# Performance work log

Hardware: AMD Instinct MI355X
Metric: run time of the kernel (lower is better)

## Reference

```python
import jax, jax.numpy as jnp
import numpy as np

B, C, H, W = 4, 128, 128, 128
_PARAM_IDS = ["1", "2", "4", "5", "7", "8", "9", "10", "12", "13", "15", "16"]


def setup_inputs() -> dict:
    key = jax.random.key(0)
    ks = jax.random.split(key, 2 + 2 * len(_PARAM_IDS))
    scale = 1.0 / np.sqrt(C).astype(np.float32)
    inp = {
        "x": jax.random.normal(ks[0], (B, C, H, W), jnp.float32),
        "y": jax.random.uniform(ks[1], (B, C, H, W), jnp.float32),  # edge gate in [0,1)
    }
    for i, n in enumerate(_PARAM_IDS):
        inp[f"w{n}"] = jax.random.normal(ks[2 + 2 * i], (C, C), jnp.float32) * scale
        inp[f"b{n}"] = jax.random.normal(ks[3 + 2 * i], (C,), jnp.float32) * scale
    return inp


def pw(t, w, b):
    # kernel-size-1 Conv1d: t [B,C,M] -> [B,C,M]
    return jnp.einsum('oc,bcm->bom', w, t) + b[None, :, None]


def gated_scan(seq_x, seq_y, wa, ba, wb, bb, relu_first):
    # seq_x, seq_y: [L, B, C, M]; recurrence h_k = relu(conv_a(x_k) + conv_b(h_{k-1}) * y_{k-1})
    first = jax.nn.relu(seq_x[0]) if relu_first else seq_x[0]

    def step(prev, inp):
        xi, yp = inp
        h = jax.nn.relu(pw(xi, wa, ba) + pw(prev, wb, bb) * yp)
        return h, h

    _, outs = jax.lax.scan(step, first, (seq_x[1:], seq_y[:-1]))
    return jnp.concatenate([first[None], outs], axis=0)


def reference(x, y, w1, b1, w2, b2, w4, b4, w5, b5, w7, b7, w8, b8,
              w9, b9, w10, b10, w12, b12, w13, b13, w15, b15, w16, b16):
    rows_x = jnp.transpose(x, (2, 0, 1, 3))   # [H,B,C,W]
    rows_y = jnp.transpose(y, (2, 0, 1, 3))   # [H,B,C,W]
    y_cols = jnp.transpose(y, (3, 0, 1, 2))   # [W,B,C,H]

    # south scan over height (row 0 untouched, no relu on it)
    hs_rows = gated_scan(rows_x, rows_y, w1, b1, w2, b2, relu_first=False)
    hs_cols = jnp.transpose(hs_rows, (3, 1, 2, 0))  # [W,B,C,H]
    # south-east / south-west scans over width (boundary column gets relu)
    hse = gated_scan(hs_cols, y_cols, w4, b4, w5, b5, relu_first=True)
    hsw = gated_scan(hs_cols[::-1], y_cols[::-1], w7, b7, w8, b8, relu_first=True)[::-1]

    # north scan over height (reversed; boundary row gets relu)
    hn_rows = gated_scan(rows_x[::-1], rows_y[::-1], w9, b9, w10, b10, relu_first=True)[::-1]
    hn_cols = jnp.transpose(hn_rows, (3, 1, 2, 0))  # [W,B,C,H]
    hne = gated_scan(hn_cols, y_cols, w12, b12, w13, b13, relu_first=True)
    hnw = gated_scan(hn_cols[::-1], y_cols[::-1], w15, b15, w16, b16, relu_first=True)[::-1]

    out_cols = hse + hsw + hne + hnw  # [W,B,C,H]
    return jnp.transpose(out_cols, (1, 2, 3, 0))  # [B,C,H,W]
```

## Files before the change

### kernel.cpp

```cpp
#include <hip/hip_runtime.h>

typedef unsigned int uint;
typedef unsigned short ushort;
typedef __attribute__((ext_vector_type(8))) short short8;
typedef __attribute__((ext_vector_type(4))) float f32x4;

#define NPOS 16384
#define PLANE 2097152
#define XR_OFF 0
#define GR_OFF 32768
#define OR_OFF 65536
#define HP_OFF 98304
#define LDS_BYTES 114688

__device__ __forceinline__ uint fbits(float a) { return __builtin_bit_cast(uint, a); }
__device__ __forceinline__ uint rnehi(float a) {
  const uint u = fbits(a);
  return (u + 0x7FFFu + ((u >> 16) & 1u)) & 0xFFFF0000u;
}
__device__ __forceinline__ float fhi(float a) { return __builtin_bit_cast(float, rnehi(a)); }
__device__ __forceinline__ uint packhi(float a, float b) { return (rnehi(a) >> 16) | rnehi(b); }
__device__ __forceinline__ uint packtr(float a, float b) {
  return (fbits(a) >> 16) | (fbits(b) & 0xFFFF0000u);
}
__device__ __forceinline__ float b2f(uint h16) { return __builtin_bit_cast(float, h16 << 16); }

__device__ __forceinline__ f32x4 MF(short8 a, short8 b, f32x4 c) {
  return __builtin_amdgcn_mfma_f32_16x16x32_bf16(a, b, c, 0, 0, 0);
}
__device__ __forceinline__ void fill16(const void* g, char* l) {
  __builtin_amdgcn_global_load_lds((const __attribute__((address_space(1))) void*)g,
                                   (__attribute__((address_space(3))) void*)l, 16, 0, 0);
}
__device__ __forceinline__ void split8(float4 v0, float4 v1, short8& hi, short8& lo) {
  union { short8 s; uint u[4]; } H, L;
  H.u[0] = packhi(v0.x, v0.y); H.u[1] = packhi(v0.z, v0.w);
  H.u[2] = packhi(v1.x, v1.y); H.u[3] = packhi(v1.z, v1.w);
  L.u[0] = packtr(v0.x - fhi(v0.x), v0.y - fhi(v0.y));
  L.u[1] = packtr(v0.z - fhi(v0.z), v0.w - fhi(v0.w));
  L.u[2] = packtr(v1.x - fhi(v1.x), v1.y - fhi(v1.y));
  L.u[3] = packtr(v1.z - fhi(v1.z), v1.w - fhi(v1.w));
  hi = H.s; lo = L.s;
}

#define BAR() asm volatile("s_waitcnt lgkmcnt(0)\n\ts_barrier" ::: "memory")


__global__ __launch_bounds__(256) void k_transpose_x(const float* __restrict__ x,
                                                     ushort* __restrict__ xhi,
                                                     ushort* __restrict__ xlo) {
  __shared__ float tile[128][129];
  const int b = blockIdx.x >> 7, h = blockIdx.x & 127;
  const int t = threadIdx.x, half = t >> 7, lane = t & 127;
  const float* src = x + (size_t)b * PLANE + (size_t)h * 128;
  for (int c0 = 0; c0 < 128; c0 += 2) {
    const int c = c0 + half;
    tile[c][lane] = src[(size_t)c * NPOS + lane];
  }
  __syncthreads();
  const int wq = t >> 6, cp = t & 63;
  for (int w0 = 0; w0 < 128; w0 += 4) {
    const int w = w0 + wq;
    const float v0 = tile[2 * cp][w], v1 = tile[2 * cp + 1][w];
    const size_t e = ((size_t)(b * 128 + w) * 128 + h) * 128 + 2 * cp;
    *(uint*)(xhi + e) = packhi(v0, v1);
    *(uint*)(xlo + e) = packtr(v0 - fhi(v0), v1 - fhi(v1));
  }
}

__global__ __launch_bounds__(256) void k_transpose_y(const float* __restrict__ y,
                                                     float* __restrict__ yt1,
                                                     float* __restrict__ yt2) {
  __shared__ float tile[128][129];
  const int b = blockIdx.x >> 7, h = blockIdx.x & 127;
  const int t = threadIdx.x, half = t >> 7, lane = t & 127;
  const float* src = y + (size_t)b * PLANE + (size_t)h * 128;
  for (int c0 = 0; c0 < 128; c0 += 2) {
    const int c = c0 + half;
    tile[c][lane] = src[(size_t)c * NPOS + lane];
  }
  __syncthreads();
  float* d1 = yt1 + (size_t)b * PLANE + (size_t)h * 128;
  float* d2 = yt2 + ((size_t)(b * 128 + h)) * NPOS;
  for (int w0 = 0; w0 < 128; w0 += 2) {
    const int w = w0 + half;
    const float v = tile[lane][w];
    d1[(size_t)w * NPOS + lane] = v;
    d2[(size_t)w * 128 + lane] = v;
  }
}

template <bool RELU0, bool REV, bool ACCUM, bool OUT16>
__device__ __forceinline__ void scan16(
    char* lds,
    const ushort* __restrict__ xhi, const ushort* __restrict__ xlo, size_t in_base,
    const float* __restrict__ gate, size_t gate_base,
    float* __restrict__ outf, ushort* __restrict__ outhi, ushort* __restrict__ outlo,
    size_t out_base, int out_ps, int out_ls,
    const float* __restrict__ Wa, const float* __restrict__ Ba,
    const float* __restrict__ Wb, const float* __restrict__ Bb) {
  const int t = threadIdx.x;
  const int wv = t >> 6, l = t & 63;
  const int line = l & 15, g4 = l >> 4;

  short8 wah[2][4], wal[2][4], wbh[2][4], wbl[2][4];
#pragma unroll
  for (int tt = 0; tt < 2; ++tt)
#pragma unroll
    for (int kt = 0; kt < 4; ++kt) {
      const int row = 32 * wv + 16 * tt + line;
      const int kc = 32 * kt + 8 * g4;
      const float4 a0 = *(const float4*)(Wa + row * 128 + kc);
      const float4 a1 = *(const float4*)(Wa + row * 128 + kc + 4);
      const float4 c0 = *(const float4*)(Wb + row * 128 + kc);
      const float4 c1 = *(const float4*)(Wb + row * 128 + kc + 4);
      split8(a0, a1, wah[tt][kt], wal[tt][kt]);
      split8(c0, c1, wbh[tt][kt], wbl[tt][kt]);
    }
  f32x4 baf[2], bbf[2];
#pragma unroll
  for (int tt = 0; tt < 2; ++tt) {
    baf[tt] = *(const f32x4*)(Ba + 32 * wv + 16 * tt + 4 * g4);
    bbf[tt] = *(const f32x4*)(Bb + 32 * wv + 16 * tt + 4 * g4);
  }

  auto P = [](int p) -> int { return REV ? 127 - p : p; };

  auto fillX = [&](int p, int slot) {
    const ushort* src = (wv >> 1) ? xlo : xhi;
#pragma unroll
    for (int kk = 0; kk < 2; ++kk) {
      const int k = 2 * (wv & 1) + kk;
      const int lf = 4 * k + g4;
      const int cf = l & 15;
      const size_t e = in_base + (size_t)lf * NPOS + (size_t)p * 128 + 8 * (cf ^ (lf & 7));
      fill16(src + e, lds + XR_OFF + slot * 8192 + (wv >> 1) * 4096 + k * 1024 + l * 16);
    }
  };
  auto fillG = [&](int p, int slot) {
#pragma unroll
    for (int kk = 0; kk < 2; ++kk) {
      const int k = 2 * wv + kk;
      const int lf = 2 * k + (l >> 5);
      const int cf = l & 31;
      const size_t e = gate_base + (size_t)lf * NPOS + (size_t)p * 128 + 4 * (cf ^ (lf & 7));
      fill16(gate + e, lds + GR_OFF + slot * 8192 + k * 1024 + l * 16);
    }
  };
  auto fillO = [&](int p, int slot) {
#pragma unroll
    for (int kk = 0; kk < 2; ++kk) {
      const int k = 2 * wv + kk;
      const int lf = 2 * k + (l >> 5);
      const int cf = l & 31;
      const size_t e = out_base + (size_t)p * out_ps + (size_t)lf * out_ls + 4 * (cf ^ (lf & 7));
      fill16(outf + e, lds + OR_OFF + slot * 8192 + k * 1024 + l * 16);
    }
  };

#pragma unroll
  for (int p = 0; p < 4; ++p) {
    fillX(P(p), p);
    fillG(P(p), p);
    if (ACCUM) fillO(P(p), p);
  }
  asm volatile("s_waitcnt vmcnt(0) lgkmcnt(0)\n\ts_barrier" ::: "memory");

  {
    const char* X0 = lds + XR_OFF;
    const char* O0 = lds + OR_OFF;
    char* Hwr = lds + HP_OFF;
#pragma unroll
    for (int tt = 0; tt < 2; ++tt) {
      const int chw = 4 * wv + 2 * tt + (g4 >> 1);
      const int boff = line * 256 + ((chw ^ (line & 7)) << 4) + 8 * (g4 & 1);
      const uint2 xh = *(const uint2*)(X0 + boff);
      const uint2 xl = *(const uint2*)(X0 + 4096 + boff);
      float4 f;
      f.x = b2f(xh.x & 0xFFFFu) + b2f(xl.x & 0xFFFFu);
      f.y = b2f(xh.x >> 16) + b2f(xl.x >> 16);
      f.z = b2f(xh.y & 0xFFFFu) + b2f(xl.y & 0xFFFFu);
      f.w = b2f(xh.y >> 16) + b2f(xl.y >> 16);
      if (RELU0) {
        f.x = fmaxf(f.x, 0.f); f.y = fmaxf(f.y, 0.f);
        f.z = fmaxf(f.z, 0.f); f.w = fmaxf(f.w, 0.f);
      }
      uint2 hw, lw;
      hw.x = packhi(f.x, f.y); hw.y = packhi(f.z, f.w);
      lw.x = packtr(f.x - fhi(f.x), f.y - fhi(f.y));
      lw.y = packtr(f.z - fhi(f.z), f.w - fhi(f.w));
      *(uint2*)(Hwr + boff) = hw;
      *(uint2*)(Hwr + 4096 + boff) = lw;
      const int ci0 = 32 * wv + 16 * tt + 4 * g4;
      const size_t oe = out_base + (size_t)P(0) * out_ps + (size_t)line * out_ls + ci0;
      if (OUT16) {
        *(uint2*)(outhi + oe) = hw;
        *(uint2*)(outlo + oe) = lw;
      } else {
        float4 o = f;
        if (ACCUM) {
          const int c32 = 8 * wv + 4 * tt + g4;
          const float4 ov = *(const float4*)(O0 + line * 512 + ((c32 ^ (line & 7)) << 4));
          o.x += ov.x; o.y += ov.y; o.z += ov.z; o.w += ov.w;
        }
        *(float4*)(outf + oe) = o;
      }
    }
  }
  BAR();

#pragma unroll 1
  for (int s = 1; s < 128; ++s) {
    if (s + 3 <= 127) {
      fillX(P(s + 3), (s + 3) & 3);
      if (ACCUM) fillO(P(s + 3), (s + 3) & 3);
    }
    if (s + 2 <= 127) fillG(P(s + 2), (s + 2) & 3);

    f32x4 accF[2], accR[2];
    accF[0] = baf[0]; accF[1] = baf[1];
    accR[0] = bbf[0]; accR[1] = bbf[1];
    const char* Hrd = lds + HP_OFF + ((s - 1) & 1) * 8192;
    const char* Xrd = lds + XR_OFF + (s & 3) * 8192;
#pragma unroll
    for (int kt = 0; kt < 4; ++kt) {
      const int ro = line * 256 + (((4 * kt + g4) ^ (line & 7)) << 4);
      const short8 hh = *(const short8*)(Hrd + ro);
      const short8 hl = *(const short8*)(Hrd + 4096 + ro);
      const short8 xh = *(const short8*)(Xrd + ro);
      const short8 xl = *(const short8*)(Xrd + 4096 + ro);
      accR[0] = MF(wbh[0][kt], hh, accR[0]);
      accR[0] = MF(wbh[0][kt], hl, accR[0]);
      accR[0] = MF(wbl[0][kt], hh, accR[0]);
      accR[1] = MF(wbh[1][kt], hh, accR[1]);
      accR[1] = MF(wbh[1][kt], hl, accR[1]);
      accR[1] = MF(wbl[1][kt], hh, accR[1]);
      accF[0] = MF(wah[0][kt], xh, accF[0]);
      accF[0] = MF(wah[0][kt], xl, accF[0]);
      accF[0] = MF(wal[0][kt], xh, accF[0]);
      accF[1] = MF(wah[1][kt], xh, accF[1]);
      accF[1] = MF(wah[1][kt], xl, accF[1]);
      accF[1] = MF(wal[1][kt], xh, accF[1]);
    }

    const char* Grd = lds + GR_OFF + ((s - 1) & 3) * 8192;
    const char* Ord = lds + OR_OFF + (s & 3) * 8192;
    char* Hwr = lds + HP_OFF + (s & 1) * 8192;
#pragma unroll
    for (int tt = 0; tt < 2; ++tt) {
      const int c32 = 8 * wv + 4 * tt + g4;
      const float4 g = *(const float4*)(Grd + line * 512 + ((c32 ^ (line & 7)) << 4));
      float4 h;
      h.x = fmaxf(fmaf(accR[tt][0], g.x, accF[tt][0]), 0.f);
      h.y = fmaxf(fmaf(accR[tt][1], g.y, accF[tt][1]), 0.f);
      h.z = fmaxf(fmaf(accR[tt][2], g.z, accF[tt][2]), 0.f);
      h.w = fmaxf(fmaf(accR[tt][3], g.w, accF[tt][3]), 0.f);
      uint2 hw, lw;
      hw.x = packhi(h.x, h.y); hw.y = packhi(h.z, h.w);
      lw.x = packtr(h.x - fhi(h.x), h.y - fhi(h.y));
      lw.y = packtr(h.z - fhi(h.z), h.w - fhi(h.w));
      const int chw = 4 * wv + 2 * tt + (g4 >> 1);
      const int wo = line * 256 + ((chw ^ (line & 7)) << 4) + 8 * (g4 & 1);
      *(uint2*)(Hwr + wo) = hw;
      *(uint2*)(Hwr + 4096 + wo) = lw;
      const int ci0 = 32 * wv + 16 * tt + 4 * g4;
      const size_t oe = out_base + (size_t)P(s) * out_ps + (size_t)line * out_ls + ci0;
      if (OUT16) {
        *(uint2*)(outhi + oe) = hw;
        *(uint2*)(outlo + oe) = lw;
      } else {
        float4 o = h;
        if (ACCUM) {
          const float4 ov = *(const float4*)(Ord + line * 512 + ((c32 ^ (line & 7)) << 4));
          o.x += ov.x; o.y += ov.y; o.z += ov.z; o.w += ov.w;
        }
        *(float4*)(outf + oe) = o;
      }
    }
    BAR();
    asm volatile("s_waitcnt vmcnt(8)" ::: "memory");
  }
}

__global__ __launch_bounds__(256, 1) void k_scan_ph1(
    const ushort* __restrict__ xhi, const ushort* __restrict__ xlo,
    const float* __restrict__ yt1,
    ushort* __restrict__ hs_hi, ushort* __restrict__ hs_lo,
    ushort* __restrict__ hn_hi, ushort* __restrict__ hn_lo,
    const float* w1, const float* b1, const float* w2, const float* b2,
    const float* w9, const float* b9, const float* w10, const float* b10) {
  __shared__ __align__(16) char lds[LDS_BYTES];
  const int id = blockIdx.x;
  const int scan = id >> 5, b = (id >> 3) & 3, wg = id & 7;
  const size_t in_base = ((size_t)(b * 128 + wg * 16)) * NPOS;
  const size_t out_base = (size_t)b * PLANE + (size_t)(wg * 16) * 128;
  if (scan == 0)
    scan16<false, false, false, true>(lds, xhi, xlo, in_base, yt1, in_base,
                                      nullptr, hs_hi, hs_lo, out_base, NPOS, 128,
                                      w1, b1, w2, b2);
  else
    scan16<true, true, false, true>(lds, xhi, xlo, in_base, yt1, in_base,
                                    nullptr, hn_hi, hn_lo, out_base, NPOS, 128,
                                    w9, b9, w10, b10);
}

__global__ __launch_bounds__(256, 1) void k_scan_ph2(
    const ushort* __restrict__ hs_hi, const ushort* __restrict__ hs_lo,
    const ushort* __restrict__ hn_hi, const ushort* __restrict__ hn_lo,
    const float* __restrict__ yt2, float* __restrict__ outA, float* __restrict__ outB,
    const float* w4, const float* b4, const float* w5, const float* b5,
    const float* w7, const float* b7, const float* w8, const float* b8,
    const float* w12, const float* b12, const float* w13, const float* b13,
    const float* w15, const float* b15, const float* w16, const float* b16) {
  __shared__ __align__(16) char lds[LDS_BYTES];
  const int id = blockIdx.x;
  const int grp = id >> 5, b = (id >> 3) & 3, hg = id & 7;
  const size_t base = ((size_t)(b * 128 + hg * 16)) * NPOS;
  const ushort* ihi = grp ? hn_hi : hs_hi;
  const ushort* ilo = grp ? hn_lo : hs_lo;
  float* o = grp ? outB : outA;
  const float* wa1 = grp ? w12 : w4; const float* ba1 = grp ? b12 : b4;
  const float* wb1 = grp ? w13 : w5; const float* bb1 = grp ? b13 : b5;
  const float* wa2 = grp ? w15 : w7; const float* ba2 = grp ? b15 : b7;
  const float* wb2 = grp ? w16 : w8; const float* bb2 = grp ? b16 : b8;
  scan16<true, false, false, false>(lds, ihi, ilo, base, yt2, base,
                                    o, nullptr, nullptr, base, 128, NPOS,
                                    wa1, ba1, wb1, bb1);
  asm volatile("s_waitcnt vmcnt(0) lgkmcnt(0)\n\ts_barrier" ::: "memory");
  scan16<true, true, true, false>(lds, ihi, ilo, base, yt2, base,
                                  o, nullptr, nullptr, base, 128, NPOS,
                                  wa2, ba2, wb2, bb2);
}

__global__ __launch_bounds__(256) void k_final(const float* __restrict__ outA,
                                               const float* __restrict__ outB,
                                               float* __restrict__ out) {
  __shared__ float tile[128][129];
  const int b = blockIdx.x >> 7, h = blockIdx.x & 127;
  const int t = threadIdx.x, half = t >> 7, lane = t & 127;
  const float* pa = outA + ((size_t)(b * 128 + h)) * NPOS;
  const float* pb = outB + ((size_t)(b * 128 + h)) * NPOS;
  for (int w0 = 0; w0 < 128; w0 += 2) {
    const int w = w0 + half;
    tile[w][lane] = pa[(size_t)w * 128 + lane] + pb[(size_t)w * 128 + lane];
  }
  __syncthreads();
  float* dst = out + (size_t)b * PLANE + (size_t)h * 128;
  for (int c0 = 0; c0 < 128; c0 += 2) {
    const int c = c0 + half;
    dst[(size_t)c * NPOS + lane] = tile[lane][c];
  }
}

extern "C" void kernel_launch(void* const* d_in, const int* in_sizes, int n_in,
                              void* d_out, int out_size, void* d_ws, size_t ws_size,
                              hipStream_t stream) {
  const float* x = (const float*)d_in[0];
  const float* y = (const float*)d_in[1];
  const float* w1 = (const float*)d_in[2];  const float* b1 = (const float*)d_in[3];
  const float* w2 = (const float*)d_in[4];  const float* b2 = (const float*)d_in[5];
  const float* w4 = (const float*)d_in[6];  const float* b4 = (const float*)d_in[7];
  const float* w5 = (const float*)d_in[8];  const float* b5 = (const float*)d_in[9];
  const float* w7 = (const float*)d_in[10]; const float* b7 = (const float*)d_in[11];
  const float* w8 = (const float*)d_in[12]; const float* b8 = (const float*)d_in[13];
  const float* w9 = (const float*)d_in[14]; const float* b9 = (const float*)d_in[15];
  const float* w10 = (const float*)d_in[16]; const float* b10 = (const float*)d_in[17];
  const float* w12 = (const float*)d_in[18]; const float* b12 = (const float*)d_in[19];
  const float* w13 = (const float*)d_in[20]; const float* b13 = (const float*)d_in[21];
  const float* w15 = (const float*)d_in[22]; const float* b15 = (const float*)d_in[23];
  const float* w16 = (const float*)d_in[24]; const float* b16 = (const float*)d_in[25];

  if (ws_size < 167772160) return;
  char* ws = (char*)d_ws;
  ushort* xt_hi = (ushort*)ws;
  ushort* xt_lo = (ushort*)(ws + 16777216);
  float* yt1 = (float*)(ws + 33554432);
  float* yt2 = (float*)(ws + 67108864);
  ushort* hs_hi = (ushort*)(ws + 100663296);
  ushort* hs_lo = (ushort*)(ws + 117440512);
  ushort* hn_hi = (ushort*)(ws + 134217728);
  ushort* hn_lo = (ushort*)(ws + 150994944);
  float* outA = (float*)ws;
  float* outB = (float*)(ws + 33554432);

  dim3 blk(256);
  k_transpose_x<<<512, blk, 0, stream>>>(x, xt_hi, xt_lo);
  k_transpose_y<<<512, blk, 0, stream>>>(y, yt1, yt2);
  k_scan_ph1<<<64, blk, 0, stream>>>(xt_hi, xt_lo, yt1, hs_hi, hs_lo, hn_hi, hn_lo,
                                     w1, b1, w2, b2, w9, b9, w10, b10);
  k_scan_ph2<<<64, blk, 0, stream>>>(hs_hi, hs_lo, hn_hi, hn_lo, yt2, outA, outB,
                                     w4, b4, w5, b5, w7, b7, w8, b8,
                                     w12, b12, w13, b13, w15, b15, w16, b16);
  k_final<<<512, blk, 0, stream>>>(outA, outB, (float*)d_out);
}
```

Before: 430.6 us.

## Remap scan LDS tiles to fragment order and tune wait counts

Staging tiles in LDS are rearranged so each lane reads its MFMA and gate/output fragments contiguously at l*16, replacing the XOR-swizzled row layout. The gate prefetch is merged with the X/O prefetch, MFMAs are interleaved across the four accumulators with raised wave priority, and per-variant vmcnt waits replace the single one. Phase-1 LDS shrinks by dropping the unused output buffer. Bank conflicts on the new layout and the exact vmcnt counts are correctness and speed risks.

```diff
diff --git a/kernel.cpp b/kernel.cpp
--- a/kernel.cpp
+++ b/kernel.cpp
@@ -9,9 +9,10 @@
 #define PLANE 2097152
 #define XR_OFF 0
 #define GR_OFF 32768
-#define OR_OFF 65536
-#define HP_OFF 98304
-#define LDS_BYTES 114688
+#define HP_OFF 65536
+#define OR_OFF 81920
+#define LDS_PH1 81920
+#define LDS_PH2 114688
 
 __device__ __forceinline__ uint fbits(float a) { return __builtin_bit_cast(uint, a); }
 __device__ __forceinline__ uint rnehi(float a) {
@@ -44,7 +45,6 @@
 }
 
 #define BAR() asm volatile("s_waitcnt lgkmcnt(0)\n\ts_barrier" ::: "memory")
-
 
 __global__ __launch_bounds__(256) void k_transpose_x(const float* __restrict__ x,
                                                      ushort* __restrict__ xhi,
@@ -110,12 +110,10 @@
     for (int kt = 0; kt < 4; ++kt) {
       const int row = 32 * wv + 16 * tt + line;
       const int kc = 32 * kt + 8 * g4;
-      const float4 a0 = *(const float4*)(Wa + row * 128 + kc);
-      const float4 a1 = *(const float4*)(Wa + row * 128 + kc + 4);
-      const float4 c0 = *(const float4*)(Wb + row * 128 + kc);
-      const float4 c1 = *(const float4*)(Wb + row * 128 + kc + 4);
-      split8(a0, a1, wah[tt][kt], wal[tt][kt]);
-      split8(c0, c1, wbh[tt][kt], wbl[tt][kt]);
+      split8(*(const float4*)(Wa + row * 128 + kc), *(const float4*)(Wa + row * 128 + kc + 4),
+             wah[tt][kt], wal[tt][kt]);
+      split8(*(const float4*)(Wb + row * 128 + kc), *(const float4*)(Wb + row * 128 + kc + 4),
+             wbh[tt][kt], wbl[tt][kt]);
     }
   f32x4 baf[2], bbf[2];
 #pragma unroll
@@ -126,56 +124,48 @@
 
   auto P = [](int p) -> int { return REV ? 127 - p : p; };
 
+  const int sp = wv >> 1;
+  const ushort* xsrc = sp ? xlo : xhi;
+  const int lf = l & 15;
+
   auto fillX = [&](int p, int slot) {
-    const ushort* src = (wv >> 1) ? xlo : xhi;
-#pragma unroll
-    for (int kk = 0; kk < 2; ++kk) {
-      const int k = 2 * (wv & 1) + kk;
-      const int lf = 4 * k + g4;
-      const int cf = l & 15;
-      const size_t e = in_base + (size_t)lf * NPOS + (size_t)p * 128 + 8 * (cf ^ (lf & 7));
-      fill16(src + e, lds + XR_OFF + slot * 8192 + (wv >> 1) * 4096 + k * 1024 + l * 16);
+#pragma unroll
+    for (int f = 0; f < 2; ++f) {
+      const int kg = 2 * (wv & 1) + f;
+      const int cc = 4 * kg + (l >> 4);
+      fill16(xsrc + in_base + (size_t)lf * NPOS + (size_t)p * 128 + 8 * cc,
+             lds + XR_OFF + slot * 8192 + sp * 4096 + kg * 1024 + l * 16);
     }
   };
   auto fillG = [&](int p, int slot) {
 #pragma unroll
-    for (int kk = 0; kk < 2; ++kk) {
-      const int k = 2 * wv + kk;
-      const int lf = 2 * k + (l >> 5);
-      const int cf = l & 31;
-      const size_t e = gate_base + (size_t)lf * NPOS + (size_t)p * 128 + 4 * (cf ^ (lf & 7));
-      fill16(gate + e, lds + GR_OFF + slot * 8192 + k * 1024 + l * 16);
-    }
+    for (int f = 0; f < 2; ++f)
+      fill16(gate + gate_base + (size_t)lf * NPOS + (size_t)p * 128 + 32 * wv + 16 * f + 4 * (l >> 4),
+             lds + GR_OFF + slot * 8192 + wv * 2048 + f * 1024 + l * 16);
   };
   auto fillO = [&](int p, int slot) {
 #pragma unroll
-    for (int kk = 0; kk < 2; ++kk) {
-      const int k = 2 * wv + kk;
-      const int lf = 2 * k + (l >> 5);
-      const int cf = l & 31;
-      const size_t e = out_base + (size_t)p * out_ps + (size_t)lf * out_ls + 4 * (cf ^ (lf & 7));
-      fill16(outf + e, lds + OR_OFF + slot * 8192 + k * 1024 + l * 16);
-    }
+    for (int f = 0; f < 2; ++f)
+      fill16(outf + out_base + (size_t)p * out_ps + (size_t)lf * out_ls + 32 * wv + 16 * f + 4 * (l >> 4),
+             lds + OR_OFF + slot * 8192 + wv * 2048 + f * 1024 + l * 16);
   };
 
 #pragma unroll
   for (int p = 0; p < 4; ++p) {
     fillX(P(p), p);
-    fillG(P(p), p);
+    if (p < 3) fillG(P(p), p);
     if (ACCUM) fillO(P(p), p);
   }
   asm volatile("s_waitcnt vmcnt(0) lgkmcnt(0)\n\ts_barrier" ::: "memory");
 
   {
-    const char* X0 = lds + XR_OFF;
-    const char* O0 = lds + OR_OFF;
     char* Hwr = lds + HP_OFF;
 #pragma unroll
     for (int tt = 0; tt < 2; ++tt) {
-      const int chw = 4 * wv + 2 * tt + (g4 >> 1);
-      const int boff = line * 256 + ((chw ^ (line & 7)) << 4) + 8 * (g4 & 1);
-      const uint2 xh = *(const uint2*)(X0 + boff);
-      const uint2 xl = *(const uint2*)(X0 + 4096 + boff);
+      const int cw = 4 * wv + 2 * tt + (g4 >> 1);
+      const int boff = (cw * 16 + line) * 16 + 8 * (g4 & 1);
+      const uint2 xh = *(const uint2*)(lds + XR_OFF + boff);
+      const uint2 xl = *(const uint2*)(lds + XR_OFF + 4096 + boff);
       float4 f;
       f.x = b2f(xh.x & 0xFFFFu) + b2f(xl.x & 0xFFFFu);
       f.y = b2f(xh.x >> 16) + b2f(xl.x >> 16);
@@ -199,9 +189,8 @@
       } else {
         float4 o = f;
         if (ACCUM) {
-          const int c32 = 8 * wv + 4 * tt + g4;
-          const float4 ov = *(const float4*)(O0 + line * 512 + ((c32 ^ (line & 7)) << 4));
-          o.x += ov.x; o.y += ov.y; o.z += ov.z; o.w += ov.w;
+          const f32x4 ov = *(const f32x4*)(lds + OR_OFF + wv * 2048 + tt * 1024 + l * 16);
+          o.x += ov[0]; o.y += ov[1]; o.z += ov[2]; o.w += ov[3];
         }
         *(float4*)(outf + oe) = o;
       }
@@ -211,58 +200,57 @@
 
 #pragma unroll 1
   for (int s = 1; s < 128; ++s) {
-    if (s + 3 <= 127) {
+    if (s <= 124) {
       fillX(P(s + 3), (s + 3) & 3);
+      fillG(P(s + 2), (s + 2) & 3);
       if (ACCUM) fillO(P(s + 3), (s + 3) & 3);
     }
-    if (s + 2 <= 127) fillG(P(s + 2), (s + 2) & 3);
-
-    f32x4 accF[2], accR[2];
-    accF[0] = baf[0]; accF[1] = baf[1];
-    accR[0] = bbf[0]; accR[1] = bbf[1];
-    const char* Hrd = lds + HP_OFF + ((s - 1) & 1) * 8192;
-    const char* Xrd = lds + XR_OFF + (s & 3) * 8192;
+
+    f32x4 aF0 = baf[0], aF1 = baf[1], aR0 = bbf[0], aR1 = bbf[1];
+    const char* H = lds + HP_OFF + ((s - 1) & 1) * 8192;
+    const char* X = lds + XR_OFF + (s & 3) * 8192;
+    __builtin_amdgcn_s_setprio(1);
 #pragma unroll
     for (int kt = 0; kt < 4; ++kt) {
-      const int ro = line * 256 + (((4 * kt + g4) ^ (line & 7)) << 4);
-      const short8 hh = *(const short8*)(Hrd + ro);
-      const short8 hl = *(const short8*)(Hrd + 4096 + ro);
-      const short8 xh = *(const short8*)(Xrd + ro);
-      const short8 xl = *(const short8*)(Xrd + 4096 + ro);
-      accR[0] = MF(wbh[0][kt], hh, accR[0]);
-      accR[0] = MF(wbh[0][kt], hl, accR[0]);
-      accR[0] = MF(wbl[0][kt], hh, accR[0]);
-      accR[1] = MF(wbh[1][kt], hh, accR[1]);
-      accR[1] = MF(wbh[1][kt], hl, accR[1]);
-      accR[1] = MF(wbl[1][kt], hh, accR[1]);
-      accF[0] = MF(wah[0][kt], xh, accF[0]);
-      accF[0] = MF(wah[0][kt], xl, accF[0]);
-      accF[0] = MF(wal[0][kt], xh, accF[0]);
-      accF[1] = MF(wah[1][kt], xh, accF[1]);
-      accF[1] = MF(wah[1][kt], xl, accF[1]);
-      accF[1] = MF(wal[1][kt], xh, accF[1]);
-    }
-
-    const char* Grd = lds + GR_OFF + ((s - 1) & 3) * 8192;
-    const char* Ord = lds + OR_OFF + (s & 3) * 8192;
+      const short8 hh = *(const short8*)(H + kt * 1024 + l * 16);
+      const short8 hl = *(const short8*)(H + 4096 + kt * 1024 + l * 16);
+      const short8 xh = *(const short8*)(X + kt * 1024 + l * 16);
+      const short8 xl = *(const short8*)(X + 4096 + kt * 1024 + l * 16);
+      aR0 = MF(wbh[0][kt], hh, aR0);
+      aR1 = MF(wbh[1][kt], hh, aR1);
+      aF0 = MF(wah[0][kt], xh, aF0);
+      aF1 = MF(wah[1][kt], xh, aF1);
+      aR0 = MF(wbh[0][kt], hl, aR0);
+      aR1 = MF(wbh[1][kt], hl, aR1);
+      aF0 = MF(wah[0][kt], xl, aF0);
+      aF1 = MF(wah[1][kt], xl, aF1);
+      aR0 = MF(wbl[0][kt], hh, aR0);
+      aR1 = MF(wbl[1][kt], hh, aR1);
+      aF0 = MF(wal[0][kt], xh, aF0);
+      aF1 = MF(wal[1][kt], xh, aF1);
+    }
+    __builtin_amdgcn_s_setprio(0);
+
+    const char* Grd = lds + GR_OFF + ((s - 1) & 3) * 8192 + wv * 2048;
+    const char* Ord = lds + OR_OFF + (s & 3) * 8192 + wv * 2048;
     char* Hwr = lds + HP_OFF + (s & 1) * 8192;
+    const f32x4 aR[2] = {aR0, aR1}, aF[2] = {aF0, aF1};
 #pragma unroll
     for (int tt = 0; tt < 2; ++tt) {
-      const int c32 = 8 * wv + 4 * tt + g4;
-      const float4 g = *(const float4*)(Grd + line * 512 + ((c32 ^ (line & 7)) << 4));
+      const f32x4 g = *(const f32x4*)(Grd + tt * 1024 + l * 16);
       float4 h;
-      h.x = fmaxf(fmaf(accR[tt][0], g.x, accF[tt][0]), 0.f);
-      h.y = fmaxf(fmaf(accR[tt][1], g.y, accF[tt][1]), 0.f);
-      h.z = fmaxf(fmaf(accR[tt][2], g.z, accF[tt][2]), 0.f);
-      h.w = fmaxf(fmaf(accR[tt][3], g.w, accF[tt][3]), 0.f);
+      h.x = fmaxf(fmaf(aR[tt][0], g[0], aF[tt][0]), 0.f);
+      h.y = fmaxf(fmaf(aR[tt][1], g[1], aF[tt][1]), 0.f);
+      h.z = fmaxf(fmaf(aR[tt][2], g[2], aF[tt][2]), 0.f);
+      h.w = fmaxf(fmaf(aR[tt][3], g[3], aF[tt][3]), 0.f);
       uint2 hw, lw;
       hw.x = packhi(h.x, h.y); hw.y = packhi(h.z, h.w);
       lw.x = packtr(h.x - fhi(h.x), h.y - fhi(h.y));
       lw.y = packtr(h.z - fhi(h.z), h.w - fhi(h.w));
-      const int chw = 4 * wv + 2 * tt + (g4 >> 1);
-      const int wo = line * 256 + ((chw ^ (line & 7)) << 4) + 8 * (g4 & 1);
-      *(uint2*)(Hwr + wo) = hw;
-      *(uint2*)(Hwr + 4096 + wo) = lw;
+      const int cw = 4 * wv + 2 * tt + (g4 >> 1);
+      const int boff = (cw * 16 + line) * 16 + 8 * (g4 & 1);
+      *(uint2*)(Hwr + boff) = hw;
+      *(uint2*)(Hwr + 4096 + boff) = lw;
       const int ci0 = 32 * wv + 16 * tt + 4 * g4;
       const size_t oe = out_base + (size_t)P(s) * out_ps + (size_t)line * out_ls + ci0;
       if (OUT16) {
@@ -271,14 +259,19 @@
       } else {
         float4 o = h;
         if (ACCUM) {
-          const float4 ov = *(const float4*)(Ord + line * 512 + ((c32 ^ (line & 7)) << 4));
-          o.x += ov.x; o.y += ov.y; o.z += ov.z; o.w += ov.w;
+          const f32x4 ov = *(const f32x4*)(Ord + tt * 1024 + l * 16);
+          o.x += ov[0]; o.y += ov[1]; o.z += ov[2]; o.w += ov[3];
         }
         *(float4*)(outf + oe) = o;
       }
     }
+    if constexpr (ACCUM)
+      asm volatile("s_waitcnt vmcnt(16)" ::: "memory");
+    else if constexpr (OUT16)
+      asm volatile("s_waitcnt vmcnt(18)" ::: "memory");
+    else
+      asm volatile("s_waitcnt vmcnt(12)" ::: "memory");
     BAR();
-    asm volatile("s_waitcnt vmcnt(8)" ::: "memory");
   }
 }
 
@@ -289,7 +282,7 @@
     ushort* __restrict__ hn_hi, ushort* __restrict__ hn_lo,
     const float* w1, const float* b1, const float* w2, const float* b2,
     const float* w9, const float* b9, const float* w10, const float* b10) {
-  __shared__ __align__(16) char lds[LDS_BYTES];
+  __shared__ __align__(16) char lds[LDS_PH1];
   const int id = blockIdx.x;
   const int scan = id >> 5, b = (id >> 3) & 3, wg = id & 7;
   const size_t in_base = ((size_t)(b * 128 + wg * 16)) * NPOS;
@@ -312,7 +305,7 @@
     const float* w7, const float* b7, const float* w8, const float* b8,
     const float* w12, const float* b12, const float* w13, const float* b13,
     const float* w15, const float* b15, const float* w16, const float* b16) {
-  __shared__ __align__(16) char lds[LDS_BYTES];
+  __shared__ __align__(16) char lds[LDS_PH2];
   const int id = blockIdx.x;
   const int grp = id >> 5, b = (id >> 3) & 3, hg = id & 7;
   const size_t base = ((size_t)(b * 128 + hg * 16)) * NPOS;
```

New measurement: 430.0 us. Within noise of the previous version (-0.1%).
